# Kernel tuning notes

Measured on AMD Instinct MI355X. Metric: run time of the kernel, lower is better.

Reference implementation:

```python
import jax, jax.numpy as jnp
import numpy as np

N_NUC = 100_000
N_NN = 1_600_000
EMB = 128
MSG = 32
OUT = 128
LN_EPS = 1e-6  # flax LayerNorm default


def setup_inputs() -> dict:
    key = jax.random.key(0)
    ks = jax.random.split(key, 12)
    inp = {
        "s_embed": jax.random.normal(ks[0], (N_NUC, EMB), jnp.float32),
        "r_embed": jax.random.normal(ks[1], (N_NUC, EMB), jnp.float32),
        "e_embed": jax.random.normal(ks[2], (N_NN, MSG), jnp.float32),
        "norm": jax.random.uniform(ks[3], (N_NUC,), jnp.float32),
        "senders": jax.random.randint(ks[4], (N_NN,), 0, N_NUC, jnp.int32),
        "receivers": jax.random.randint(ks[5], (N_NN,), 0, N_NUC, jnp.int32),
        # learned parameters
        "W_s": jax.random.normal(ks[6], (EMB, MSG), jnp.float32) / np.sqrt(EMB),
        "b_s": jnp.zeros((MSG,), jnp.float32),
        "W_r": jax.random.normal(ks[7], (EMB, MSG), jnp.float32) / np.sqrt(EMB),
        "b_r": jnp.zeros((MSG,), jnp.float32),
        "ln_scale": jnp.ones((MSG,), jnp.float32),
        "ln_bias": jnp.zeros((MSG,), jnp.float32),
        "W_e": jax.random.normal(ks[8], (MSG, MSG), jnp.float32) / np.sqrt(MSG),
        "W_out": jax.random.normal(ks[9], (MSG, OUT), jnp.float32) / np.sqrt(MSG),
    }
    return inp


def _layernorm(x, scale, bias):
    mu = jnp.mean(x, axis=-1, keepdims=True)
    var = jnp.mean(jnp.square(x - mu), axis=-1, keepdims=True)
    return (x - mu) * jax.lax.rsqrt(var + LN_EPS) * scale + bias


def reference(s_embed, r_embed, e_embed, norm, senders, receivers,
              W_s, b_s, W_r, b_r, ln_scale, ln_bias, W_e, W_out):
    # Dense projections on nodes, then gather per edge: [n_nn, msg]
    inp = (s_embed @ W_s + b_s)[senders] + (r_embed @ W_r + b_r)[receivers]
    inp = _layernorm(inp, ln_scale, ln_bias)
    inp = jax.nn.silu(inp)
    inp = inp * (e_embed @ W_e)  # elementwise edge gating
    # scatter-add to receivers: [n_nuc, msg]
    msg = jax.ops.segment_sum(inp, receivers, num_segments=s_embed.shape[0])
    msg = msg * norm[:, None]
    return jax.nn.silu(msg @ W_out)
```

## Files before the change

kernel.cpp:

```cpp
#include <hip/hip_runtime.h>
#include <hip/hip_bf16.h>
#include <math.h>

#define N_NUC_C 100000
#define N_NN_C  1600000
#define EMB_C   128
#define MSG_C   32
#define OUT_C   128
#define NB1     98
#define NPART   8
#define R_PER_P (N_NUC_C / NPART)
#define SBLK    784
#define STHREADS (SBLK * 256)
#define LDS_USTR 17
#define RANK_BLOCKS 6250
#define PROJ_BLOCKS 1564

typedef __attribute__((ext_vector_type(8))) short bf16x8;
typedef __attribute__((ext_vector_type(4))) float f32x4;

__device__ __forceinline__ float silu_f(float y) {
    return y / (1.0f + __expf(-y));
}

__device__ __forceinline__ unsigned pack_bf16x2(float a, float b) {
    unsigned ua = __float_as_uint(a); ua += 0x7FFFu + ((ua >> 16) & 1u);
    unsigned ub = __float_as_uint(b); ub += 0x7FFFu + ((ub >> 16) & 1u);
    return (ua >> 16) | (ub & 0xFFFF0000u);
}

__device__ __forceinline__ unsigned short bf16_of(float a) {
    unsigned ua = __float_as_uint(a); ua += 0x7FFFu + ((ua >> 16) & 1u);
    return (unsigned short)(ua >> 16);
}

__device__ __forceinline__ void proj_body(
    int n, int pr, int c0,
    const float* __restrict__ s_embed, const float* __restrict__ r_embed,
    const float* __restrict__ W_s, const float* __restrict__ b_s,
    const float* __restrict__ W_r, const float* __restrict__ b_r,
    float* __restrict__ proj)
{
    const float* __restrict__ src = pr ? r_embed : s_embed;
    const float* __restrict__ W   = pr ? W_r : W_s;
    const float* __restrict__ b   = pr ? b_r : b_s;
    float* __restrict__ dst = proj + (size_t)pr * N_NUC_C * MSG_C;

    float acc[16];
    #pragma unroll
    for (int i = 0; i < 16; ++i) acc[i] = b[c0 + i];

    const float* row = src + (size_t)n * EMB_C;
    #pragma unroll 4
    for (int k = 0; k < EMB_C; k += 4) {
        const float4 rv = *reinterpret_cast<const float4*>(row + k);
        #pragma unroll
        for (int i = 0; i < 16; ++i) {
            acc[i] = fmaf(rv.x, W[(k + 0) * MSG_C + c0 + i], acc[i]);
            acc[i] = fmaf(rv.y, W[(k + 1) * MSG_C + c0 + i], acc[i]);
            acc[i] = fmaf(rv.z, W[(k + 2) * MSG_C + c0 + i], acc[i]);
            acc[i] = fmaf(rv.w, W[(k + 3) * MSG_C + c0 + i], acc[i]);
        }
    }

    float4* d = reinterpret_cast<float4*>(dst + (size_t)n * MSG_C + c0);
    d[0] = make_float4(acc[0],  acc[1],  acc[2],  acc[3]);
    d[1] = make_float4(acc[4],  acc[5],  acc[6],  acc[7]);
    d[2] = make_float4(acc[8],  acc[9],  acc[10], acc[11]);
    d[3] = make_float4(acc[12], acc[13], acc[14], acc[15]);
}

__global__ __launch_bounds__(256) void proj_rank_kernel(
    const float* __restrict__ s_embed, const float* __restrict__ r_embed,
    const float* __restrict__ W_s, const float* __restrict__ b_s,
    const float* __restrict__ W_r, const float* __restrict__ b_r,
    float* __restrict__ proj,
    const int* __restrict__ receivers, int* __restrict__ cnt,
    int* __restrict__ rank)
{
    const int bid = blockIdx.x;
    if (bid < RANK_BLOCKS) {
        const int e = bid * 256 + threadIdx.x;
        if (e < N_NN_C) rank[e] = atomicAdd(&cnt[receivers[e]], 1);
        return;
    }
    const int pb  = bid - RANK_BLOCKS;
    const int sub = pb & 3;
    const int n   = (pb >> 2) * 256 + threadIdx.x;
    if (n >= N_NUC_C) return;
    proj_body(n, sub >> 1, (sub & 1) * 16,
              s_embed, r_embed, W_s, b_s, W_r, b_r, proj);
}

__global__ __launch_bounds__(256) void proj_kernel(
    const float* __restrict__ s_embed, const float* __restrict__ r_embed,
    const float* __restrict__ W_s, const float* __restrict__ b_s,
    const float* __restrict__ W_r, const float* __restrict__ b_r,
    float* __restrict__ proj)
{
    const int n = blockIdx.x * blockDim.x + threadIdx.x;
    if (n >= N_NUC_C) return;
    const int sub = blockIdx.y;
    proj_body(n, sub >> 1, (sub & 1) * 16,
              s_embed, r_embed, W_s, b_s, W_r, b_r, proj);
}

__global__ __launch_bounds__(256) void scan1_kernel(
    const int* __restrict__ cnt, int* __restrict__ excl, int* __restrict__ blockTot)
{
    __shared__ int waveTot[4];
    const int t = threadIdx.x, b = blockIdx.x;
    const int lane = t & 63, wid = t >> 6;
    const int base = b * 1024 + t * 4;

    int d0 = (base + 0 < N_NUC_C) ? cnt[base + 0] : 0;
    int d1 = (base + 1 < N_NUC_C) ? cnt[base + 1] : 0;
    int d2 = (base + 2 < N_NUC_C) ? cnt[base + 2] : 0;
    int d3 = (base + 3 < N_NUC_C) ? cnt[base + 3] : 0;
    const int s = d0 + d1 + d2 + d3;

    int incl = s;
    #pragma unroll
    for (int off = 1; off < 64; off <<= 1) {
        int v = __shfl_up(incl, off);
        if (lane >= off) incl += v;
    }
    const int wexcl = incl - s;
    if (lane == 63) waveTot[wid] = incl;
    __syncthreads();
    int wbase = 0;
    for (int w = 0; w < wid; ++w) wbase += waveTot[w];
    const int e0 = wbase + wexcl;

    if (base + 0 < N_NUC_C) excl[base + 0] = e0;
    if (base + 1 < N_NUC_C) excl[base + 1] = e0 + d0;
    if (base + 2 < N_NUC_C) excl[base + 2] = e0 + d0 + d1;
    if (base + 3 < N_NUC_C) excl[base + 3] = e0 + d0 + d1 + d2;
    if (t == 255) blockTot[b] = wbase + incl;
}

__global__ __launch_bounds__(128) void scan2_kernel(
    const int* __restrict__ blockTot, int* __restrict__ blockOff)
{
    __shared__ int sh[128];
    const int t = threadIdx.x;
    const int v = (t < NB1) ? blockTot[t] : 0;
    sh[t] = v;
    __syncthreads();
    #pragma unroll
    for (int off = 1; off < 128; off <<= 1) {
        int x = 0;
        if (t >= off) x = sh[t - off];
        __syncthreads();
        sh[t] += x;
        __syncthreads();
    }
    if (t < NB1) blockOff[t] = sh[t] - v;
}

__global__ __launch_bounds__(256) void scan3_kernel(
    const int* __restrict__ excl, const int* __restrict__ blockOff,
    int* __restrict__ offsets)
{
    const int n = blockIdx.x * blockDim.x + threadIdx.x;
    if (n < N_NUC_C) offsets[n] = excl[n] + blockOff[n >> 10];
    if (n == 0) offsets[N_NUC_C] = N_NN_C;
}

__global__ __launch_bounds__(256) void scatter_pack8_kernel(
    const int* __restrict__ senders, const int* __restrict__ receivers,
    const int* __restrict__ rank, const int* __restrict__ offsets,
    int4* __restrict__ edge_pack)
{
    const int p    = blockIdx.x & 7;
    const int blk  = blockIdx.x >> 3;
    const int base = blk * 256 + threadIdx.x;
    const int rlo  = p * R_PER_P;
    const int rhi  = rlo + R_PER_P;

    #pragma unroll
    for (int k = 0; k < 8; ++k) {
        const int e = base + k * STHREADS;
        if (e < N_NN_C) {
            const int r = receivers[e];
            if (r >= rlo && r < rhi) {
                const int dst = offsets[r] + rank[e];
                edge_pack[dst] = make_int4(e, senders[e], r, 0);
            }
        }
    }
}

__global__ __launch_bounds__(256) void fused_csr_kernel(
    const float* __restrict__ proj,
    const float* __restrict__ e_embed,
    const int4*  __restrict__ edge_pack,
    const int*   __restrict__ offsets,
    const float* __restrict__ ln_scale,
    const float* __restrict__ ln_bias,
    const float* __restrict__ W_e,
    float*       __restrict__ msg)
{
    __shared__ unsigned lds_ev[256 * LDS_USTR];
    __shared__ unsigned lds_g [256 * LDS_USTR];
    __shared__ int      lds_r[256];

    const int t    = threadIdx.x;
    const int lane = t & 63;
    const int wb   = t & ~63;
    const int B0   = blockIdx.x * 256;

    const int4 pk = edge_pack[B0 + t];
    const int e = pk.x, s = pk.y, r = pk.z;
    lds_r[t] = r;

    {
        const float4* ee = reinterpret_cast<const float4*>(e_embed + (size_t)e * MSG_C);
        unsigned* evrow = &lds_ev[t * LDS_USTR];
        #pragma unroll
        for (int q = 0; q < 8; ++q) {
            const float4 v = ee[q];
            evrow[2*q+0] = pack_bf16x2(v.x, v.y);
            evrow[2*q+1] = pack_bf16x2(v.z, v.w);
        }
    }

    bf16x8 bf0, bf1;
    {
        const int kg = (lane >> 4) * 8;
        const int n0 = lane & 15;
        #pragma unroll
        for (int i = 0; i < 8; ++i) {
            bf0[i] = (short)bf16_of(W_e[(kg + i) * MSG_C + n0]);
            bf1[i] = (short)bf16_of(W_e[(kg + i) * MSG_C + 16 + n0]);
        }
    }

    __syncthreads();

    {
        unsigned short* g16 = reinterpret_cast<unsigned short*>(lds_g);
        #pragma unroll
        for (int mt = 0; mt < 4; ++mt) {
            const int arow = wb + mt * 16 + (lane & 15);
            const unsigned* ar = &lds_ev[arow * LDS_USTR + ((lane >> 4) << 2)];
            union { unsigned u[4]; bf16x8 v; } cvt;
            cvt.u[0] = ar[0]; cvt.u[1] = ar[1]; cvt.u[2] = ar[2]; cvt.u[3] = ar[3];
            const bf16x8 af = cvt.v;
            f32x4 z = {0.f, 0.f, 0.f, 0.f};
            const f32x4 a0 = __builtin_amdgcn_mfma_f32_16x16x32_bf16(af, bf0, z, 0, 0, 0);
            const f32x4 a1 = __builtin_amdgcn_mfma_f32_16x16x32_bf16(af, bf1, z, 0, 0, 0);
            const int rbase = wb + mt * 16 + ((lane >> 4) << 2);
            #pragma unroll
            for (int rg = 0; rg < 4; ++rg) {
                g16[(rbase + rg) * (2 * LDS_USTR) + (lane & 15)]      = bf16_of(a0[rg]);
                g16[(rbase + rg) * (2 * LDS_USTR) + 16 + (lane & 15)] = bf16_of(a1[rg]);
            }
        }
    }

    __syncthreads();

    float g[MSG_C];
    {
        const unsigned* gr = &lds_g[t * LDS_USTR];
        #pragma unroll
        for (int j = 0; j < 16; ++j) {
            const unsigned u = gr[j];
            g[2*j]   = __uint_as_float(u << 16);
            g[2*j+1] = __uint_as_float(u & 0xFFFF0000u);
        }
    }

    const float4* ps = reinterpret_cast<const float4*>(proj + (size_t)s * MSG_C);
    const float4* pq = reinterpret_cast<const float4*>(proj + (size_t)(N_NUC_C + r) * MSG_C);
    float x[MSG_C];
    #pragma unroll
    for (int q = 0; q < 8; ++q) {
        const float4 a = ps[q];
        const float4 b = pq[q];
        x[4*q+0] = a.x + b.x; x[4*q+1] = a.y + b.y;
        x[4*q+2] = a.z + b.z; x[4*q+3] = a.w + b.w;
    }

    float mu = 0.0f;
    #pragma unroll
    for (int c = 0; c < MSG_C; ++c) mu += x[c];
    mu *= (1.0f / MSG_C);
    float var = 0.0f;
    #pragma unroll
    for (int c = 0; c < MSG_C; ++c) { const float d = x[c] - mu; var = fmaf(d, d, var); }
    var *= (1.0f / MSG_C);
    const float rs = rsqrtf(var + 1e-6f);

    unsigned* orow = &lds_ev[t * LDS_USTR];
    #pragma unroll
    for (int i = 0; i < 16; ++i) {
        const int c0_ = 2*i, c1_ = 2*i + 1;
        const float y0 = (x[c0_] - mu) * rs * ln_scale[c0_] + ln_bias[c0_];
        const float y1 = (x[c1_] - mu) * rs * ln_scale[c1_] + ln_bias[c1_];
        orow[i] = pack_bf16x2(silu_f(y0) * g[c0_], silu_f(y1) * g[c1_]);
    }

    __syncthreads();

    const int r0 = lds_r[0];
    const int r1 = lds_r[255];
    const int total = (r1 - r0 + 1) << 5;

    for (int p = t; p < total; p += 256) {
        const int n  = r0 + (p >> 5);
        const int ch = p & 31;
        int b  = offsets[n];
        int en = offsets[n + 1];
        const bool interior = (b >= B0) && (en <= B0 + 256);
        if (b < B0) b = B0;
        if (en > B0 + 256) en = B0 + 256;

        const int dw  = ch >> 1;
        const bool hi = (ch & 1);
        float sum = 0.0f;
        for (int q = b - B0; q < en - B0; ++q) {
            const unsigned u = lds_ev[q * LDS_USTR + dw];
            sum += __uint_as_float(hi ? (u & 0xFFFF0000u) : (u << 16));
        }

        float* dst = msg + (size_t)n * MSG_C + ch;
        if (interior)       *dst = sum;
        else if (en > b)    atomicAdd(dst, sum);
    }
}

__global__ __launch_bounds__(256) void edge_kernel(
    const float* __restrict__ proj, const float* __restrict__ e_embed,
    const int* __restrict__ senders, const int* __restrict__ receivers,
    const float* __restrict__ ln_scale, const float* __restrict__ ln_bias,
    const float* __restrict__ W_e, float* __restrict__ msg)
{
    const int e = blockIdx.x * blockDim.x + threadIdx.x;
    if (e >= N_NN_C) return;
    const int s = senders[e];
    const int r = receivers[e];
    const float4* ps = reinterpret_cast<const float4*>(proj + (size_t)s * MSG_C);
    const float4* pq = reinterpret_cast<const float4*>(proj + (size_t)(N_NUC_C + r) * MSG_C);
    float x[MSG_C];
    #pragma unroll
    for (int q = 0; q < 8; ++q) {
        const float4 a = ps[q];
        const float4 b = pq[q];
        x[4*q+0] = a.x + b.x; x[4*q+1] = a.y + b.y;
        x[4*q+2] = a.z + b.z; x[4*q+3] = a.w + b.w;
    }
    float mu = 0.0f;
    #pragma unroll
    for (int c = 0; c < MSG_C; ++c) mu += x[c];
    mu *= (1.0f / MSG_C);
    float var = 0.0f;
    #pragma unroll
    for (int c = 0; c < MSG_C; ++c) { const float d = x[c] - mu; var = fmaf(d, d, var); }
    var *= (1.0f / MSG_C);
    const float rs = rsqrtf(var + 1e-6f);
    #pragma unroll
    for (int c = 0; c < MSG_C; ++c) {
        const float y = (x[c] - mu) * rs * ln_scale[c] + ln_bias[c];
        x[c] = silu_f(y);
    }
    float ev[MSG_C];
    const float4* ee = reinterpret_cast<const float4*>(e_embed + (size_t)e * MSG_C);
    #pragma unroll
    for (int q = 0; q < 8; ++q) {
        const float4 v = ee[q];
        ev[4*q+0] = v.x; ev[4*q+1] = v.y; ev[4*q+2] = v.z; ev[4*q+3] = v.w;
    }
    float g[MSG_C];
    #pragma unroll
    for (int c = 0; c < MSG_C; ++c) g[c] = 0.0f;
    #pragma unroll
    for (int k = 0; k < MSG_C; ++k) {
        const float ek = ev[k];
        #pragma unroll
        for (int c = 0; c < MSG_C; ++c) g[c] = fmaf(ek, W_e[k * MSG_C + c], g[c]);
    }
    float* mrow = msg + (size_t)r * MSG_C;
    #pragma unroll
    for (int c = 0; c < MSG_C; ++c) atomicAdd(mrow + c, x[c] * g[c]);
}

__global__ __launch_bounds__(256) void out_kernel(
    const float* __restrict__ msg, const float* __restrict__ norm,
    const float* __restrict__ W_out, float* __restrict__ out)
{
    const int j     = threadIdx.x & (OUT_C - 1);
    const int local = threadIdx.x >> 7;

    float w[MSG_C];
    #pragma unroll
    for (int k = 0; k < MSG_C; ++k) w[k] = W_out[k * OUT_C + j];

    for (int n = blockIdx.x * 2 + local; n < N_NUC_C; n += gridDim.x * 2) {
        const float4* m4 = reinterpret_cast<const float4*>(msg + (size_t)n * MSG_C);
        float acc = 0.0f;
        #pragma unroll
        for (int q = 0; q < 8; ++q) {
            const float4 mv = m4[q];
            acc = fmaf(mv.x, w[4*q+0], acc);
            acc = fmaf(mv.y, w[4*q+1], acc);
            acc = fmaf(mv.z, w[4*q+2], acc);
            acc = fmaf(mv.w, w[4*q+3], acc);
        }
        acc *= norm[n];
        out[(size_t)n * OUT_C + j] = silu_f(acc);
    }
}

extern "C" void kernel_launch(void* const* d_in, const int* in_sizes, int n_in,
                              void* d_out, int out_size, void* d_ws, size_t ws_size,
                              hipStream_t stream) {
    const float* s_embed   = (const float*)d_in[0];
    const float* r_embed   = (const float*)d_in[1];
    const float* e_embed   = (const float*)d_in[2];
    const float* norm      = (const float*)d_in[3];
    const int*   senders   = (const int*)d_in[4];
    const int*   receivers = (const int*)d_in[5];
    const float* W_s       = (const float*)d_in[6];
    const float* b_s       = (const float*)d_in[7];
    const float* W_r       = (const float*)d_in[8];
    const float* b_r       = (const float*)d_in[9];
    const float* ln_scale  = (const float*)d_in[10];
    const float* ln_bias   = (const float*)d_in[11];
    const float* W_e       = (const float*)d_in[12];
    const float* W_out     = (const float*)d_in[13];
    float* out = (float*)d_out;

    char* ws = (char*)d_ws;
    size_t off = 0;
    auto alloc = [&](size_t bytes) { char* p = ws + off; off += (bytes + 255) & ~(size_t)255; return p; };

    float* proj      = (float*)alloc((size_t)2 * N_NUC_C * MSG_C * 4);
    float* msg       = (float*)alloc((size_t)N_NUC_C * MSG_C * 4);
    const size_t off_min = off;
    int*   cnt       = (int*)  alloc((size_t)N_NUC_C * 4);
    int*   excl      = (int*)  alloc((size_t)N_NUC_C * 4);
    int*   offsets   = (int*)  alloc((size_t)(N_NUC_C + 1) * 4);
    int*   blockTot  = (int*)  alloc(128 * 4);
    int*   blockOff  = (int*)  alloc(128 * 4);
    int*   rank      = (int*)  alloc((size_t)N_NN_C * 4);
    int4*  edge_pack = (int4*) alloc((size_t)N_NN_C * 16);
    const size_t off_full = off;

    if (off_full <= ws_size) {
        hipMemsetAsync(cnt, 0, (size_t)N_NUC_C * 4, stream);
        hipMemsetAsync(msg, 0, (size_t)N_NUC_C * MSG_C * 4, stream);
        proj_rank_kernel<<<RANK_BLOCKS + PROJ_BLOCKS, 256, 0, stream>>>(
            s_embed, r_embed, W_s, b_s, W_r, b_r, proj, receivers, cnt, rank);
        scan1_kernel<<<NB1, 256, 0, stream>>>(cnt, excl, blockTot);
        scan2_kernel<<<1, 128, 0, stream>>>(blockTot, blockOff);
        scan3_kernel<<<(N_NUC_C + 255) / 256, 256, 0, stream>>>(excl, blockOff, offsets);
        scatter_pack8_kernel<<<NPART * SBLK, 256, 0, stream>>>(
            senders, receivers, rank, offsets, edge_pack);
        fused_csr_kernel<<<N_NN_C / 256, 256, 0, stream>>>(
            proj, e_embed, edge_pack, offsets, ln_scale, ln_bias, W_e, msg);
    } else if (off_min <= ws_size) {
        dim3 pgrid((N_NUC_C + 255) / 256, 4);
        proj_kernel<<<pgrid, 256, 0, stream>>>(s_embed, r_embed, W_s, b_s, W_r, b_r, proj);
        hipMemsetAsync(msg, 0, (size_t)N_NUC_C * MSG_C * 4, stream);
        edge_kernel<<<(N_NN_C + 255) / 256, 256, 0, stream>>>(
            proj, e_embed, senders, receivers, ln_scale, ln_bias, W_e, msg);
    }

    out_kernel<<<2048, 256, 0, stream>>>(msg, norm, W_out, out);
}
```

Baseline: 344.7 us.

## Replace global atomic rank counting with chunked LDS histograms plus per-chunk prefix scan

Instead of one global atomicAdd per edge into a 100k-entry count array, edges are split into 32 chunks and 8 receiver partitions. Each block builds a local histogram in shared memory and records a local rank per edge. A new chunkscan kernel turns the per-chunk counts into per-receiver prefix offsets and totals. The scatter then combines offset, chunk prefix and local rank. This trades contended global atomics for LDS atomics, at the cost of each hist block reading its whole chunk for every partition, a 12.8MB count matrix, and one extra kernel launch.

```diff
diff --git a/kernel.cpp b/kernel.cpp
--- a/kernel.cpp
+++ b/kernel.cpp
@@ -13,7 +13,10 @@
 #define SBLK    784
 #define STHREADS (SBLK * 256)
 #define LDS_USTR 17
-#define RANK_BLOCKS 6250
+#define NCH     32
+#define CHUNK   (N_NN_C / NCH)
+#define CH_ITERS ((CHUNK + 255) / 256)
+#define HIST_BLOCKS (NCH * NPART)
 #define PROJ_BLOCKS 1564
 
 typedef __attribute__((ext_vector_type(8))) short bf16x8;
@@ -70,21 +73,43 @@
     d[3] = make_float4(acc[12], acc[13], acc[14], acc[15]);
 }
 
-__global__ __launch_bounds__(256) void proj_rank_kernel(
+__global__ __launch_bounds__(256) void proj_hist_kernel(
     const float* __restrict__ s_embed, const float* __restrict__ r_embed,
     const float* __restrict__ W_s, const float* __restrict__ b_s,
     const float* __restrict__ W_r, const float* __restrict__ b_r,
     float* __restrict__ proj,
-    const int* __restrict__ receivers, int* __restrict__ cnt,
-    int* __restrict__ rank)
-{
+    const int* __restrict__ receivers,
+    int* __restrict__ lrank, int* __restrict__ cnt2 )
+{
+    __shared__ int cl[R_PER_P];
     const int bid = blockIdx.x;
-    if (bid < RANK_BLOCKS) {
-        const int e = bid * 256 + threadIdx.x;
-        if (e < N_NN_C) rank[e] = atomicAdd(&cnt[receivers[e]], 1);
+
+    if (bid < HIST_BLOCKS) {
+        const int c   = bid >> 3;
+        const int p   = bid & 7;
+        const int rlo = p * R_PER_P;
+
+        for (int i = threadIdx.x; i < R_PER_P; i += 256) cl[i] = 0;
+        __syncthreads();
+
+        const int ebase = c * CHUNK;
+        for (int it = 0; it < CH_ITERS; ++it) {
+            const int el = it * 256 + threadIdx.x;
+            if (el < CHUNK) {
+                const int e = ebase + el;
+                const int rr = receivers[e] - rlo;
+                if ((unsigned)rr < (unsigned)R_PER_P)
+                    lrank[e] = atomicAdd(&cl[rr], 1);
+            }
+        }
+        __syncthreads();
+
+        int* dst = cnt2 + (size_t)c * N_NUC_C + rlo;
+        for (int i = threadIdx.x; i < R_PER_P; i += 256) dst[i] = cl[i];
         return;
     }
-    const int pb  = bid - RANK_BLOCKS;
+
+    const int pb  = bid - HIST_BLOCKS;
     const int sub = pb & 3;
     const int n   = (pb >> 2) * 256 + threadIdx.x;
     if (n >= N_NUC_C) return;
@@ -103,6 +128,22 @@
     const int sub = blockIdx.y;
     proj_body(n, sub >> 1, (sub & 1) * 16,
               s_embed, r_embed, W_s, b_s, W_r, b_r, proj);
+}
+
+__global__ __launch_bounds__(256) void chunkscan_kernel(
+    int* __restrict__ cnt2, int* __restrict__ cnt)
+{
+    const int r = blockIdx.x * 256 + threadIdx.x;
+    if (r >= N_NUC_C) return;
+    int s = 0;
+    #pragma unroll
+    for (int c = 0; c < NCH; ++c) {
+        int* p = cnt2 + (size_t)c * N_NUC_C + r;
+        const int t = *p;
+        *p = s;
+        s += t;
+    }
+    cnt[r] = s;
 }
 
 __global__ __launch_bounds__(256) void scan1_kernel(
@@ -169,8 +210,8 @@
 
 __global__ __launch_bounds__(256) void scatter_pack8_kernel(
     const int* __restrict__ senders, const int* __restrict__ receivers,
-    const int* __restrict__ rank, const int* __restrict__ offsets,
-    int4* __restrict__ edge_pack)
+    const int* __restrict__ lrank, const int* __restrict__ cnt2,
+    const int* __restrict__ offsets, int4* __restrict__ edge_pack)
 {
     const int p    = blockIdx.x & 7;
     const int blk  = blockIdx.x >> 3;
@@ -184,7 +225,8 @@
         if (e < N_NN_C) {
             const int r = receivers[e];
             if (r >= rlo && r < rhi) {
-                const int dst = offsets[r] + rank[e];
+                const int c   = e / CHUNK;
+                const int dst = offsets[r] + cnt2[(size_t)c * N_NUC_C + r] + lrank[e];
                 edge_pack[dst] = make_int4(e, senders[e], r, 0);
             }
         }
@@ -444,20 +486,21 @@
     int*   offsets   = (int*)  alloc((size_t)(N_NUC_C + 1) * 4);
     int*   blockTot  = (int*)  alloc(128 * 4);
     int*   blockOff  = (int*)  alloc(128 * 4);
-    int*   rank      = (int*)  alloc((size_t)N_NN_C * 4);
+    int*   lrank     = (int*)  alloc((size_t)N_NN_C * 4);
+    int*   cnt2      = (int*)  alloc((size_t)NCH * N_NUC_C * 4);
     int4*  edge_pack = (int4*) alloc((size_t)N_NN_C * 16);
     const size_t off_full = off;
 
     if (off_full <= ws_size) {
-        hipMemsetAsync(cnt, 0, (size_t)N_NUC_C * 4, stream);
         hipMemsetAsync(msg, 0, (size_t)N_NUC_C * MSG_C * 4, stream);
-        proj_rank_kernel<<<RANK_BLOCKS + PROJ_BLOCKS, 256, 0, stream>>>(
-            s_embed, r_embed, W_s, b_s, W_r, b_r, proj, receivers, cnt, rank);
+        proj_hist_kernel<<<HIST_BLOCKS + PROJ_BLOCKS, 256, 0, stream>>>(
+            s_embed, r_embed, W_s, b_s, W_r, b_r, proj, receivers, lrank, cnt2);
+        chunkscan_kernel<<<(N_NUC_C + 255) / 256, 256, 0, stream>>>(cnt2, cnt);
         scan1_kernel<<<NB1, 256, 0, stream>>>(cnt, excl, blockTot);
         scan2_kernel<<<1, 128, 0, stream>>>(blockTot, blockOff);
         scan3_kernel<<<(N_NUC_C + 255) / 256, 256, 0, stream>>>(excl, blockOff, offsets);
         scatter_pack8_kernel<<<NPART * SBLK, 256, 0, stream>>>(
-            senders, receivers, rank, offsets, edge_pack);
+            senders, receivers, lrank, cnt2, offsets, edge_pack);
         fused_csr_kernel<<<N_NN_C / 256, 256, 0, stream>>>(
             proj, e_embed, edge_pack, offsets, ln_scale, ln_bias, W_e, msg);
     } else if (off_min <= ws_size) {
```

Result: slower. 366.6 us (+6.3%).
